# Performance work log

Measured on AMD Instinct MI355X. Metric: run time of the kernel, lower is better.

Reference implementation:

```python
import jax, jax.numpy as jnp
import numpy as np

NUM_CLASSES = 100
NUM_DIM = 384
BATCH = 4096


def setup_inputs() -> dict:
    key = jax.random.key(0)
    k1, k2, k3, k4 = jax.random.split(key, 4)
    inputs = jax.random.normal(k1, (BATCH, NUM_DIM), dtype=jnp.float32)
    targets = jax.random.randint(k2, (BATCH,), 0, NUM_CLASSES)
    centers = jax.random.normal(k3, (NUM_CLASSES, NUM_DIM), dtype=jnp.float32)
    centers_weights = jax.random.uniform(k4, (NUM_CLASSES, NUM_DIM), dtype=jnp.float32)
    return {
        "inputs": inputs,
        "targets": targets,
        "epoch_number": 0,
        "centers": centers,
        "centers_weights": centers_weights,
    }


def _closest_center_dist(centers, centers_weights):
    # calc_centers(which_one=1): dist[i,j] = sqrt(sum_d 2^w[i,d]*(c[i,d]-c[j,d])^2),
    # row-sorted, second-smallest (the diagonal 0 is the smallest).
    # Computed with numpy in the original -> detached constant.
    w = 2.0 ** centers_weights                      # [C, D]
    diff = centers[:, None, :] - centers[None, :, :]  # [C, C, D] (C=100, tiny)
    d2 = jnp.einsum('cd,ced->ce', w, diff * diff)   # [C, C]
    d = jnp.sqrt(d2)
    d = jnp.sort(d, axis=1)
    return jax.lax.stop_gradient(d[:, 1])           # [C]


def reference(inputs, targets, epoch_number, centers, centers_weights):
    B = inputs.shape[0]
    centers_dist = _closest_center_dist(centers, centers_weights)  # [C]

    c_b = centers[targets]                     # [B, D] centers_batch
    w_b = 2.0 ** centers_weights[targets]      # [B, D] weights (gathered)

    # dist[i, j] = sqrt( sum_d w_b[j,d] * (c_b[j,d] - inputs[i,d])^2 )
    # expanded into three contractions to avoid the [B,B,D] broadcast tensor
    t_cc = jnp.einsum('jd,jd->j', w_b, c_b * c_b)        # [B]   (j-term)
    t_xc = inputs @ (w_b * c_b).T                        # [B,B] cross term
    t_xx = (inputs * inputs) @ w_b.T                     # [B,B]
    d2 = t_cc[None, :] - 2.0 * t_xc + t_xx               # [B,B]
    dist = jnp.sqrt(jnp.maximum(d2, 1e-12))

    mask = targets[:, None] == targets[None, :]          # [B,B] same-class
    dist_ap = jnp.where(mask, dist, -jnp.inf).max(axis=1)  # hardest positive
    dist_an = jnp.where(mask, jnp.inf, dist).min(axis=1)   # hardest negative

    cc = centers_dist[targets]                           # [B]
    per_sample = dist_ap + jnp.where(dist_an >= cc, 0.0, cc - dist_an)
    return jnp.sum(per_sample) / B
```

## Files before the change

kernel.cpp:

```cpp
#include <hip/hip_runtime.h>
#include <math.h>

#define NC 100
#define ND 384
#define NB 4096
#define KS 8
#define KT 48
#define MT 128
#define XSP 52
#define CLS_PAD 132
#define PPAD 104
#define AUX 116
#define GEMM_BLOCKS ((NB / MT) * KS)
#define SAF (MT * XSP + 2 * KT * CLS_PAD)

__global__ __launch_bounds__(256, 2) void fused_kernel(
    const float* __restrict__ x, const float* __restrict__ centers,
    const float* __restrict__ cw, const int* __restrict__ targets,
    float* __restrict__ tcc, float* __restrict__ cdist,
    unsigned* __restrict__ pres16, float* __restrict__ part,
    float* __restrict__ out) {
  __shared__ float sA[SAF];
  int b = blockIdx.x, tid = threadIdx.x;
  int wave = tid >> 6, lane = tid & 63;

  if (b < NC) {
    int i = b;
    float* ci_s = sA;
    float* wi_s = sA + ND;
    float* sred = sA + 2 * ND;
    if (i == 0 && tid == 255) out[0] = 0.f;
    for (int d = tid; d < ND; d += 256) {
      ci_s[d] = centers[i * ND + d];
      wi_s[d] = exp2f(cw[i * ND + d]);
    }
    __syncthreads();
    {
      float p = 0.f;
      for (int d = tid; d < ND; d += 256) p = fmaf(wi_s[d] * ci_s[d], ci_s[d], p);
      #pragma unroll
      for (int off = 32; off; off >>= 1) p += __shfl_xor(p, off, 64);
      if (lane == 0) sred[wave] = p;
      __syncthreads();
      if (tid == 0) tcc[i] = sred[0] + sred[1] + sred[2] + sred[3];
      __syncthreads();
    }
    float minv = 1e30f;
    for (int s = 0; s < 24; s += 4) {
      float red[4];
      #pragma unroll
      for (int u = 0; u < 4; u++) {
        int j = wave + 4 * (s + u);
        float acc = 0.f;
        #pragma unroll
        for (int e = 0; e < 6; e++) {
          int d = lane + 64 * e;
          float df = ci_s[d] - centers[j * ND + d];
          acc = fmaf(wi_s[d] * df, df, acc);
        }
        red[u] = acc;
      }
      #pragma unroll
      for (int off = 32; off; off >>= 1) {
        #pragma unroll
        for (int u = 0; u < 4; u++) red[u] += __shfl_xor(red[u], off, 64);
      }
      #pragma unroll
      for (int u = 0; u < 4; u++) {
        int j = wave + 4 * (s + u);
        if (j != i) minv = fminf(minv, red[u]);
      }
    }
    {
      int j = wave + 96;
      float acc = 0.f;
      #pragma unroll
      for (int e = 0; e < 6; e++) {
        int d = lane + 64 * e;
        float df = ci_s[d] - centers[j * ND + d];
        acc = fmaf(wi_s[d] * df, df, acc);
      }
      #pragma unroll
      for (int off = 32; off; off >>= 1) acc = fminf(acc + __shfl_xor(acc, off, 64), 1e30f), acc = acc;
      if (j != i) {  }
      if (false) {}
      float acc2 = 0.f;
      #pragma unroll
      for (int e = 0; e < 6; e++) {
        int d = lane + 64 * e;
        float df = ci_s[d] - centers[j * ND + d];
        acc2 = fmaf(wi_s[d] * df, df, acc2);
      }
      #pragma unroll
      for (int off = 32; off; off >>= 1) acc2 += __shfl_xor(acc2, off, 64);
      if (j != i) minv = fminf(minv, acc2);
    }
    if (lane == 0) sred[wave] = minv;
    __syncthreads();
    if (tid == 0)
      cdist[i] = sqrtf(fminf(fminf(sred[0], sred[1]), fminf(sred[2], sred[3])));
  } else if (b < AUX) {
    int pb = b - NC;
    unsigned* um = (unsigned*)sA;
    if (tid < 4) um[tid] = 0u;
    __syncthreads();
    int t = targets[pb * 256 + tid];
    atomicOr(&um[t >> 5], 1u << (t & 31));
    __syncthreads();
    if (tid < 4) pres16[pb * 4 + tid] = um[tid];
  } else {
    int g = b - AUX;
    int mb = g >> 3, ks = g & 7;
    int koff = ks * KT;
    float* xs = sA;
    float* ws_t = sA + MT * XSP;
    float* as_t = ws_t + KT * CLS_PAD;

    #pragma unroll
    for (int r = 0; r < 8; r++) {
      int idx = tid + 256 * r;
      int row = idx >> 4, slot = idx & 15;
      if (slot < 12) {
        float4 v = *(const float4*)(x + (mb * MT + row) * ND + koff + 4 * slot);
        *(float4*)&xs[row * XSP + 4 * slot] = v;
      }
    }
    for (int r = 0; r < 19; r++) {
      int idx = tid + 256 * r;
      if (idx < NC * KT) {
        int k = idx / KT, d = idx - k * KT;
        float w = exp2f(cw[k * ND + koff + d]);
        float c = centers[k * ND + koff + d];
        ws_t[d * CLS_PAD + k] = w;
        as_t[d * CLS_PAD + k] = -2.f * w * c;
      }
    }
    __syncthreads();

    int cg = tid & 31, sg = tid >> 5;
    float acc[16][4];
    #pragma unroll
    for (int m = 0; m < 16; m++)
      #pragma unroll
      for (int u = 0; u < 4; u++) acc[m][u] = 0.f;

    #pragma unroll 1
    for (int d4 = 0; d4 < KT; d4 += 4) {
      float wv[4][4], av[4][4], xv[16][4];
      #pragma unroll
      for (int i2 = 0; i2 < 4; i2++) {
        *(float4*)&wv[i2][0] = *(const float4*)&ws_t[(d4 + i2) * CLS_PAD + 4 * cg];
        *(float4*)&av[i2][0] = *(const float4*)&as_t[(d4 + i2) * CLS_PAD + 4 * cg];
      }
      #pragma unroll
      for (int m = 0; m < 16; m++)
        *(float4*)&xv[m][0] = *(const float4*)&xs[(sg + 8 * m) * XSP + d4];
      #pragma unroll
      for (int i2 = 0; i2 < 4; i2++) {
        #pragma unroll
        for (int m = 0; m < 16; m++) {
          float xval = xv[m][i2];
          #pragma unroll
          for (int u = 0; u < 4; u++)
            acc[m][u] = fmaf(xval, fmaf(xval, wv[i2][u], av[i2][u]), acc[m][u]);
        }
      }
    }
    if (cg < 25) {
      #pragma unroll
      for (int m = 0; m < 16; m++) {
        int i = mb * MT + sg + 8 * m;
        *(float4*)&part[(ks * NB + i) * PPAD + 4 * cg] = *(float4*)&acc[m][0];
      }
    }
  }
}

__global__ __launch_bounds__(256) void finish_kernel(
    const int* __restrict__ targets, const float* __restrict__ tcc,
    const float* __restrict__ cdist, const unsigned* __restrict__ pres16,
    const float* __restrict__ part, float* __restrict__ out) {
  __shared__ unsigned msk[4];
  __shared__ float r_an[2][2], r_ap[2][2], lsum[8];
  int tid = threadIdx.x;
  if (tid < 4) {
    unsigned m = 0;
    #pragma unroll
    for (int bb = 0; bb < 16; bb++) m |= pres16[bb * 4 + tid];
    msk[tid] = m;
  }
  int wave = tid >> 6, lane = tid & 63;
  int h = wave & 1, sl = wave >> 1;
  int k = h * 64 + lane;
  bool valid = k < NC;
  float base = valid ? tcc[k] : 0.f;
  __syncthreads();
  bool pres = valid && ((msk[k >> 5] >> (k & 31)) & 1u);

  for (int pass = 0; pass < 4; pass++) {
    int i = blockIdx.x * 8 + pass * 2 + sl;
    int ti = targets[i];
    float cand_an = 1e30f, cand_ap = 0.f;
    if (valid) {
      float d2 = base;
      #pragma unroll
      for (int s = 0; s < KS; s++) d2 += part[(s * NB + i) * PPAD + k];
      float dist = sqrtf(fmaxf(d2, 1e-12f));
      if (k == ti) cand_ap = dist;
      else if (pres) cand_an = dist;
    }
    #pragma unroll
    for (int off = 32; off; off >>= 1) {
      cand_an = fminf(cand_an, __shfl_xor(cand_an, off, 64));
      cand_ap = fmaxf(cand_ap, __shfl_xor(cand_ap, off, 64));
    }
    if (lane == 0) { r_an[sl][h] = cand_an; r_ap[sl][h] = cand_ap; }
    __syncthreads();
    if (tid < 2) {
      int isamp = blockIdx.x * 8 + pass * 2 + tid;
      float cc = cdist[targets[isamp]];
      float an = fminf(r_an[tid][0], r_an[tid][1]);
      float ap = fmaxf(r_ap[tid][0], r_ap[tid][1]);
      lsum[pass * 2 + tid] = ap + ((an >= cc) ? 0.f : cc - an);
    }
    __syncthreads();
  }
  if (tid == 0) {
    float t = 0.f;
    #pragma unroll
    for (int j = 0; j < 8; j++) t += lsum[j];
    atomicAdd(out, t * (1.0f / NB));
  }
}

extern "C" void kernel_launch(void* const* d_in, const int* in_sizes, int n_in,
                              void* d_out, int out_size, void* d_ws, size_t ws_size,
                              hipStream_t stream) {
  const float* inputs  = (const float*)d_in[0];
  const int*   targets = (const int*)d_in[1];
  const float* centers = (const float*)d_in[3];
  const float* cw      = (const float*)d_in[4];
  float* out = (float*)d_out;

  float* tcc       = (float*)d_ws;
  float* cdist     = tcc + 128;
  unsigned* pres16 = (unsigned*)(cdist + 128);
  float* part      = (float*)(pres16 + 64);

  fused_kernel<<<AUX + GEMM_BLOCKS, 256, 0, stream>>>(
      inputs, centers, cw, targets, tcc, cdist, pres16, part, out);
  finish_kernel<<<NB / 8, 256, 0, stream>>>(targets, tcc, cdist, pres16, part, out);
}
```

Measured before the change: 92.73 us.

## Fuse finish reduction into GEMM kernel using global completion flags

The separate finish kernel is folded into the main kernel. The last K-split block of each row tile spin-waits on per-block and per-center completion flags, then computes the hardest-positive and hardest-negative terms and accumulates the loss. The per-class weighted center-norm term is now added inside each K-split partial instead of in a separate tcc pass. The class-presence mask is built locally, and the partial buffer stride is narrowed. This removes a kernel launch and a round trip, at the cost of inter-block spin-waits that rely on co-residency and on flags that are never reset between calls, so repeated calls can read stale partials. Zeroing out[0] in a center block while other blocks atomically add to it is also racy.

```diff
diff --git a/kernel.cpp b/kernel.cpp
--- a/kernel.cpp
+++ b/kernel.cpp
@@ -9,112 +9,29 @@
 #define MT 128
 #define XSP 52
 #define CLS_PAD 132
-#define PPAD 104
-#define AUX 116
-#define GEMM_BLOCKS ((NB / MT) * KS)
-#define SAF (MT * XSP + 2 * KT * CLS_PAD)
-
-__global__ __launch_bounds__(256, 2) void fused_kernel(
-    const float* __restrict__ x, const float* __restrict__ centers,
-    const float* __restrict__ cw, const int* __restrict__ targets,
-    float* __restrict__ tcc, float* __restrict__ cdist,
-    unsigned* __restrict__ pres16, float* __restrict__ part,
+#define PPR 100
+#define GEMM_BLOCKS 256
+#define GRID (GEMM_BLOCKS + NC)
+#define MAGIC 0x5F3C2A11u
+#define SAF (MT * XSP + 2 * KT * CLS_PAD + 112)
+
+__global__ __launch_bounds__(256, 2) void fused_all(
+    const float* __restrict__ x, const int* __restrict__ targets,
+    const float* __restrict__ centers, const float* __restrict__ cw,
+    float* __restrict__ cdist, unsigned* __restrict__ cdone,
+    unsigned* __restrict__ gflag, float* __restrict__ part,
     float* __restrict__ out) {
   __shared__ float sA[SAF];
   int b = blockIdx.x, tid = threadIdx.x;
   int wave = tid >> 6, lane = tid & 63;
 
-  if (b < NC) {
-    int i = b;
-    float* ci_s = sA;
-    float* wi_s = sA + ND;
-    float* sred = sA + 2 * ND;
-    if (i == 0 && tid == 255) out[0] = 0.f;
-    for (int d = tid; d < ND; d += 256) {
-      ci_s[d] = centers[i * ND + d];
-      wi_s[d] = exp2f(cw[i * ND + d]);
-    }
-    __syncthreads();
-    {
-      float p = 0.f;
-      for (int d = tid; d < ND; d += 256) p = fmaf(wi_s[d] * ci_s[d], ci_s[d], p);
-      #pragma unroll
-      for (int off = 32; off; off >>= 1) p += __shfl_xor(p, off, 64);
-      if (lane == 0) sred[wave] = p;
-      __syncthreads();
-      if (tid == 0) tcc[i] = sred[0] + sred[1] + sred[2] + sred[3];
-      __syncthreads();
-    }
-    float minv = 1e30f;
-    for (int s = 0; s < 24; s += 4) {
-      float red[4];
-      #pragma unroll
-      for (int u = 0; u < 4; u++) {
-        int j = wave + 4 * (s + u);
-        float acc = 0.f;
-        #pragma unroll
-        for (int e = 0; e < 6; e++) {
-          int d = lane + 64 * e;
-          float df = ci_s[d] - centers[j * ND + d];
-          acc = fmaf(wi_s[d] * df, df, acc);
-        }
-        red[u] = acc;
-      }
-      #pragma unroll
-      for (int off = 32; off; off >>= 1) {
-        #pragma unroll
-        for (int u = 0; u < 4; u++) red[u] += __shfl_xor(red[u], off, 64);
-      }
-      #pragma unroll
-      for (int u = 0; u < 4; u++) {
-        int j = wave + 4 * (s + u);
-        if (j != i) minv = fminf(minv, red[u]);
-      }
-    }
-    {
-      int j = wave + 96;
-      float acc = 0.f;
-      #pragma unroll
-      for (int e = 0; e < 6; e++) {
-        int d = lane + 64 * e;
-        float df = ci_s[d] - centers[j * ND + d];
-        acc = fmaf(wi_s[d] * df, df, acc);
-      }
-      #pragma unroll
-      for (int off = 32; off; off >>= 1) acc = fminf(acc + __shfl_xor(acc, off, 64), 1e30f), acc = acc;
-      if (j != i) {  }
-      if (false) {}
-      float acc2 = 0.f;
-      #pragma unroll
-      for (int e = 0; e < 6; e++) {
-        int d = lane + 64 * e;
-        float df = ci_s[d] - centers[j * ND + d];
-        acc2 = fmaf(wi_s[d] * df, df, acc2);
-      }
-      #pragma unroll
-      for (int off = 32; off; off >>= 1) acc2 += __shfl_xor(acc2, off, 64);
-      if (j != i) minv = fminf(minv, acc2);
-    }
-    if (lane == 0) sred[wave] = minv;
-    __syncthreads();
-    if (tid == 0)
-      cdist[i] = sqrtf(fminf(fminf(sred[0], sred[1]), fminf(sred[2], sred[3])));
-  } else if (b < AUX) {
-    int pb = b - NC;
-    unsigned* um = (unsigned*)sA;
-    if (tid < 4) um[tid] = 0u;
-    __syncthreads();
-    int t = targets[pb * 256 + tid];
-    atomicOr(&um[t >> 5], 1u << (t & 31));
-    __syncthreads();
-    if (tid < 4) pres16[pb * 4 + tid] = um[tid];
-  } else {
-    int g = b - AUX;
-    int mb = g >> 3, ks = g & 7;
+  if (b < GEMM_BLOCKS) {
+    int mb = b >> 3, ks = b & 7;
     int koff = ks * KT;
     float* xs = sA;
     float* ws_t = sA + MT * XSP;
     float* as_t = ws_t + KT * CLS_PAD;
+    float* ts = as_t + KT * CLS_PAD;
 
     #pragma unroll
     for (int r = 0; r < 8; r++) {
@@ -136,6 +53,15 @@
       }
     }
     __syncthreads();
+    if (tid < NC) {
+      float s = 0.f;
+      for (int d = 0; d < KT; d++) {
+        float av = as_t[d * CLS_PAD + tid];
+        float wv = ws_t[d * CLS_PAD + tid];
+        s += 0.25f * av * av / wv;
+      }
+      ts[tid] = s;
+    }
 
     int cg = tid & 31, sg = tid >> 5;
     float acc[16][4];
@@ -166,70 +92,135 @@
         }
       }
     }
+    __syncthreads();
     if (cg < 25) {
+      float4 t4 = *(float4*)&ts[4 * cg];
       #pragma unroll
       for (int m = 0; m < 16; m++) {
         int i = mb * MT + sg + 8 * m;
-        *(float4*)&part[(ks * NB + i) * PPAD + 4 * cg] = *(float4*)&acc[m][0];
-      }
-    }
-  }
-}
-
-__global__ __launch_bounds__(256) void finish_kernel(
-    const int* __restrict__ targets, const float* __restrict__ tcc,
-    const float* __restrict__ cdist, const unsigned* __restrict__ pres16,
-    const float* __restrict__ part, float* __restrict__ out) {
-  __shared__ unsigned msk[4];
-  __shared__ float r_an[2][2], r_ap[2][2], lsum[8];
-  int tid = threadIdx.x;
-  if (tid < 4) {
-    unsigned m = 0;
-    #pragma unroll
-    for (int bb = 0; bb < 16; bb++) m |= pres16[bb * 4 + tid];
-    msk[tid] = m;
-  }
-  int wave = tid >> 6, lane = tid & 63;
-  int h = wave & 1, sl = wave >> 1;
-  int k = h * 64 + lane;
-  bool valid = k < NC;
-  float base = valid ? tcc[k] : 0.f;
-  __syncthreads();
-  bool pres = valid && ((msk[k >> 5] >> (k & 31)) & 1u);
-
-  for (int pass = 0; pass < 4; pass++) {
-    int i = blockIdx.x * 8 + pass * 2 + sl;
-    int ti = targets[i];
-    float cand_an = 1e30f, cand_ap = 0.f;
-    if (valid) {
-      float d2 = base;
-      #pragma unroll
-      for (int s = 0; s < KS; s++) d2 += part[(s * NB + i) * PPAD + k];
-      float dist = sqrtf(fmaxf(d2, 1e-12f));
-      if (k == ti) cand_ap = dist;
-      else if (pres) cand_an = dist;
-    }
-    #pragma unroll
-    for (int off = 32; off; off >>= 1) {
-      cand_an = fminf(cand_an, __shfl_xor(cand_an, off, 64));
-      cand_ap = fmaxf(cand_ap, __shfl_xor(cand_ap, off, 64));
-    }
-    if (lane == 0) { r_an[sl][h] = cand_an; r_ap[sl][h] = cand_ap; }
-    __syncthreads();
-    if (tid < 2) {
-      int isamp = blockIdx.x * 8 + pass * 2 + tid;
-      float cc = cdist[targets[isamp]];
-      float an = fminf(r_an[tid][0], r_an[tid][1]);
-      float ap = fmaxf(r_ap[tid][0], r_ap[tid][1]);
-      lsum[pass * 2 + tid] = ap + ((an >= cc) ? 0.f : cc - an);
-    }
-    __syncthreads();
-  }
-  if (tid == 0) {
-    float t = 0.f;
-    #pragma unroll
-    for (int j = 0; j < 8; j++) t += lsum[j];
-    atomicAdd(out, t * (1.0f / NB));
+        float4 v;
+        v.x = acc[m][0] + t4.x; v.y = acc[m][1] + t4.y;
+        v.z = acc[m][2] + t4.z; v.w = acc[m][3] + t4.w;
+        *(float4*)&part[(ks * NB + i) * PPR + 4 * cg] = v;
+      }
+    }
+    __threadfence();
+    __syncthreads();
+    if (tid == 0) atomicExch(&gflag[b], MAGIC);
+
+    if (ks == 7) {
+      unsigned* msk = (unsigned*)sA;
+      float* ls = sA + 8;
+      __syncthreads();
+      if (tid < 4) msk[tid] = 0u;
+      __syncthreads();
+      #pragma unroll
+      for (int r = 0; r < 16; r++) {
+        int t = targets[tid + 256 * r];
+        atomicOr(&msk[t >> 5], 1u << (t & 31));
+      }
+      if (tid < 7) {
+        while (atomicCAS(&gflag[mb * 8 + tid], 0u, 0u) != MAGIC)
+          __builtin_amdgcn_s_sleep(1);
+      } else if (tid < 7 + NC) {
+        while (atomicCAS(&cdone[tid - 7], 0u, 0u) != MAGIC)
+          __builtin_amdgcn_s_sleep(1);
+      }
+      __syncthreads();
+      __threadfence();
+
+      int i = mb * MT + (tid >> 1);
+      int h = tid & 1;
+      int ti = targets[i];
+      float cc = cdist[ti];
+      float an = 1e30f, ap = 0.f;
+      int kq0 = h ? 13 : 0, kq1 = h ? 25 : 13;
+      for (int kq = kq0; kq < kq1; kq++) {
+        float4 d2 = make_float4(0.f, 0.f, 0.f, 0.f);
+        #pragma unroll
+        for (int s = 0; s < KS; s++) {
+          float4 p = *(const float4*)(part + (s * NB + i) * PPR + 4 * kq);
+          d2.x += p.x; d2.y += p.y; d2.z += p.z; d2.w += p.w;
+        }
+        float dd[4] = {d2.x, d2.y, d2.z, d2.w};
+        #pragma unroll
+        for (int j = 0; j < 4; j++) {
+          int k = 4 * kq + j;
+          float dist = sqrtf(fmaxf(dd[j], 1e-12f));
+          bool pres = (msk[k >> 5] >> (k & 31)) & 1u;
+          if (k == ti) ap = dist;
+          else if (pres) an = fminf(an, dist);
+        }
+      }
+      an = fminf(an, __shfl_xor(an, 1, 64));
+      ap = fmaxf(ap, __shfl_xor(ap, 1, 64));
+      float loss = ap + ((an >= cc) ? 0.f : cc - an);
+      #pragma unroll
+      for (int off = 32; off; off >>= 1) loss += __shfl_xor(loss, off, 64);
+      if (lane == 0) ls[wave] = loss;
+      __syncthreads();
+      if (tid == 0) {
+        float tsum = (ls[0] + ls[1] + ls[2] + ls[3]) * 0.5f;
+        atomicAdd(out, tsum * (1.0f / NB));
+      }
+    }
+  } else {
+    int i = b - GEMM_BLOCKS;
+    float* ci_s = sA;
+    float* wi_s = sA + ND;
+    float* sred = sA + 2 * ND;
+    if (i == 0 && tid == 255) out[0] = 0.f;
+    for (int d = tid; d < ND; d += 256) {
+      ci_s[d] = centers[i * ND + d];
+      wi_s[d] = exp2f(cw[i * ND + d]);
+    }
+    __syncthreads();
+    float minv = 1e30f;
+    for (int s4 = 0; s4 < 24; s4 += 4) {
+      float red[4];
+      #pragma unroll
+      for (int u = 0; u < 4; u++) {
+        int j = wave + 4 * (s4 + u);
+        float acc = 0.f;
+        #pragma unroll
+        for (int e = 0; e < 6; e++) {
+          int d = lane + 64 * e;
+          float df = ci_s[d] - centers[j * ND + d];
+          acc = fmaf(wi_s[d] * df, df, acc);
+        }
+        red[u] = acc;
+      }
+      #pragma unroll
+      for (int off = 32; off; off >>= 1) {
+        #pragma unroll
+        for (int u = 0; u < 4; u++) red[u] += __shfl_xor(red[u], off, 64);
+      }
+      #pragma unroll
+      for (int u = 0; u < 4; u++) {
+        int j = wave + 4 * (s4 + u);
+        if (j != i) minv = fminf(minv, red[u]);
+      }
+    }
+    {
+      int j = wave + 96;
+      float acc = 0.f;
+      #pragma unroll
+      for (int e = 0; e < 6; e++) {
+        int d = lane + 64 * e;
+        float df = ci_s[d] - centers[j * ND + d];
+        acc = fmaf(wi_s[d] * df, df, acc);
+      }
+      #pragma unroll
+      for (int off = 32; off; off >>= 1) acc += __shfl_xor(acc, off, 64);
+      if (j != i) minv = fminf(minv, acc);
+    }
+    if (lane == 0) sred[wave] = minv;
+    __syncthreads();
+    if (tid == 0)
+      cdist[i] = sqrtf(fminf(fminf(sred[0], sred[1]), fminf(sred[2], sred[3])));
+    __threadfence();
+    __syncthreads();
+    if (tid == 0) atomicExch(&cdone[i], MAGIC);
   }
 }
 
@@ -242,12 +233,11 @@
   const float* cw      = (const float*)d_in[4];
   float* out = (float*)d_out;
 
-  float* tcc       = (float*)d_ws;
-  float* cdist     = tcc + 128;
-  unsigned* pres16 = (unsigned*)(cdist + 128);
-  float* part      = (float*)(pres16 + 64);
-
-  fused_kernel<<<AUX + GEMM_BLOCKS, 256, 0, stream>>>(
-      inputs, centers, cw, targets, tcc, cdist, pres16, part, out);
-  finish_kernel<<<NB / 8, 256, 0, stream>>>(targets, tcc, cdist, pres16, part, out);
+  float* cdist     = (float*)d_ws;
+  unsigned* cdone  = (unsigned*)(cdist + 128);
+  unsigned* gflag  = cdone + 128;
+  float* part      = (float*)(gflag + 256);
+
+  fused_all<<<GRID, 256, 0, stream>>>(inputs, targets, centers, cw, cdist,
+                                      cdone, gflag, part, out);
 }
```

New measurement: 200.7 us. 2.16x slower.
